# Optimization experiments

Hardware: AMD Instinct MI355X
Metric: run time of the kernel (lower is better)

The kernel has to match this reference:

```python
import jax, jax.numpy as jnp
import numpy as np

NEG_SLOPE = 0.2
EPS = 1e-16  # PyG softmax denominator epsilon


def _gatv2_layer(x, src, dst, n_nodes, W_l, W_r, att, bias):
    """Single-head GATv2Conv (PyG defaults, self loops already in src/dst).
    x: [N, F_in]; src/dst: [E]; W_l/W_r: [F_in, F_out]; att: [F_out]; bias: [F_out].
    """
    x_l = x @ W_l                       # source transform [N, F_out]
    x_r = x @ W_r                       # target transform [N, F_out]
    # per-edge attention logit: a^T LeakyReLU(x_l[j] + x_r[i])
    e = jax.nn.leaky_relu(x_l[src] + x_r[dst], NEG_SLOPE) @ att  # [E]
    # softmax over incoming edges of each destination node
    e_max = jax.ops.segment_max(e, dst, num_segments=n_nodes)    # [N]
    ex = jnp.exp(e - e_max[dst])                                  # [E]
    denom = jax.ops.segment_sum(ex, dst, num_segments=n_nodes)   # [N]
    alpha = ex / (denom[dst] + EPS)                               # [E]
    out = jax.ops.segment_sum(alpha[:, None] * x_l[src], dst, num_segments=n_nodes)
    return out + bias


def setup_inputs() -> dict:
    key = jax.random.key(0)
    N, E = 50000, 800000
    IN, HID, OUT = 128, 64, 64
    ks = jax.random.split(key, 12)
    x = jax.random.normal(ks[0], (N, IN), dtype=jnp.float32)
    edge_index = jax.random.randint(ks[1], (2, E), 0, N, dtype=jnp.int64)
    s1 = float(1.0 / np.sqrt(IN))
    s2 = float(1.0 / np.sqrt(HID))
    return {
        "x": x,
        "edge_index": edge_index,
        "W1_l": jax.random.uniform(ks[2], (IN, HID), jnp.float32, -s1, s1),
        "W1_r": jax.random.uniform(ks[3], (IN, HID), jnp.float32, -s1, s1),
        "att1": jax.random.uniform(ks[4], (HID,), jnp.float32, -s2, s2),
        "b1": jnp.zeros((HID,), jnp.float32),
        "W2_l": jax.random.uniform(ks[5], (HID, OUT), jnp.float32, -s2, s2),
        "W2_r": jax.random.uniform(ks[6], (HID, OUT), jnp.float32, -s2, s2),
        "att2": jax.random.uniform(ks[7], (OUT,), jnp.float32, -s2, s2),
        "b2": jnp.zeros((OUT,), jnp.float32),
    }


def reference(x, edge_index, W1_l, W1_r, att1, b1, W2_l, W2_r, att2, b2):
    n = x.shape[0]
    loop = jnp.arange(n, dtype=edge_index.dtype)
    src = jnp.concatenate([edge_index[0], loop])  # add self loops (PyG default)
    dst = jnp.concatenate([edge_index[1], loop])
    h = _gatv2_layer(x, src, dst, n, W1_l, W1_r, att1, b1)
    h = jax.nn.relu(h)
    out = _gatv2_layer(h, src, dst, n, W2_l, W2_r, att2, b2)
    return out
```

## Files before the change

### kernel.cpp

```cpp
#include <hip/hip_runtime.h>
#include <math.h>

#define NEG_SLOPE 0.2f
#define EPSV 1e-16f
#define NEG_HUGE -1e30f
#define CAP 64
#define GB 2048

typedef short short8 __attribute__((ext_vector_type(8)));
typedef float f32x4 __attribute__((ext_vector_type(4)));
typedef unsigned short u16;


__global__ __launch_bounds__(256) void k_wpack(
        const float* __restrict__ W1l, const float* __restrict__ W1r,
        const float* __restrict__ W2l, const float* __restrict__ W2r,
        u16* __restrict__ w1hi, u16* __restrict__ w1lo,
        u16* __restrict__ w2hi, u16* __restrict__ w2lo,
        int* __restrict__ cnt, u16* __restrict__ csrc, int N, int NP) {
    const int idx = blockIdx.x * 256 + threadIdx.x;
    const int G = gridDim.x * 256;
    const int CN = 8 * NP;
    for (int i = idx; i < CN; i += G) {
        const int cls = i / NP;
        const int r = i - cls * NP;
        const int d = r * 8 + cls;
        cnt[i] = (d < N) ? 1 : 0;
    }
    for (int d = idx; d < N; d += G) csrc[(size_t)d * CAP] = (u16)d;
    const int T1 = 128 * 128, T2 = 64 * 128;
    if (idx >= T1 + T2) return;
    u16 *dhi, *dlo; const float *Wl, *Wr; int li;
    if (idx < T1) { dhi = w1hi; dlo = w1lo; Wl = W1l; Wr = W1r; li = idx; }
    else          { dhi = w2hi; dlo = w2lo; Wl = W2l; Wr = W2r; li = idx - T1; }
    const int j = li & 7, l = (li >> 3) & 63, t = (li >> 9) & 7, c = li >> 12;
    const int k = c * 32 + (l >> 4) * 8 + j;
    const int n = t * 16 + (l & 15);
    const float v = (n < 64) ? Wl[k * 64 + n] : Wr[k * 64 + (n - 64)];
    const unsigned u = __float_as_uint(v);
    dhi[li] = (u16)(u >> 16);
    const float hif = __uint_as_float(u & 0xffff0000u);
    dlo[li] = (u16)(__float_as_uint(v - hif) >> 16);
}

__device__ __forceinline__ void split8(const float* fs, short8& ahi, short8& alo) {
#pragma unroll
    for (int j = 0; j < 8; ++j) {
        const unsigned u = __float_as_uint(fs[j]);
        ahi[j] = (short)(u >> 16);
        const float hif = __uint_as_float(u & 0xffff0000u);
        alo[j] = (short)(__float_as_uint(fs[j] - hif) >> 16);
    }
}

template <int K>
__device__ __forceinline__ void gemm_mfma_tile(const float* __restrict__ X,
                                               const u16* __restrict__ whi,
                                               const u16* __restrict__ wlo,
                                               float* __restrict__ xl,
                                               float* __restrict__ xr,
                                               int N, int tile) {
    const int lane = threadIdx.x & 63;
    const int w = threadIdx.x >> 6;
    const int rowbase = tile * 64 + w * 16;
    const int m = lane & 15, q = lane >> 4;
    int ar = rowbase + m; if (ar > N - 1) ar = N - 1;
    const float* arow = X + (size_t)ar * K + q * 8;
    f32x4 acc[8];
#pragma unroll
    for (int t = 0; t < 8; ++t) acc[t] = (f32x4){0.f, 0.f, 0.f, 0.f};
#pragma unroll
    for (int c = 0; c < K / 32; ++c) {
        const float4 f0 = *(const float4*)(arow + c * 32);
        const float4 f1 = *(const float4*)(arow + c * 32 + 4);
        const float fs[8] = {f0.x, f0.y, f0.z, f0.w, f1.x, f1.y, f1.z, f1.w};
        short8 ahi, alo;
        split8(fs, ahi, alo);
        const u16* bp = whi + ((size_t)(c * 8) * 64 + lane) * 8;
        const u16* bq = wlo + ((size_t)(c * 8) * 64 + lane) * 8;
#pragma unroll
        for (int t = 0; t < 8; ++t) {
            const short8 bhi = *(const short8*)(bp + t * 64 * 8);
            const short8 blo = *(const short8*)(bq + t * 64 * 8);
            acc[t] = __builtin_amdgcn_mfma_f32_16x16x32_bf16(bhi, ahi, acc[t], 0, 0, 0);
            acc[t] = __builtin_amdgcn_mfma_f32_16x16x32_bf16(blo, ahi, acc[t], 0, 0, 0);
            acc[t] = __builtin_amdgcn_mfma_f32_16x16x32_bf16(bhi, alo, acc[t], 0, 0, 0);
        }
    }
    const int row = rowbase + m;
    if (row < N) {
#pragma unroll
        for (int t = 0; t < 8; ++t) {
            const int colb = t * 16 + q * 4;
            float4 v;
            v.x = acc[t][0]; v.y = acc[t][1]; v.z = acc[t][2]; v.w = acc[t][3];
            float* dstp = (t < 4) ? (xl + (size_t)row * 64 + colb)
                                  : (xr + (size_t)row * 64 + (colb - 64));
            *(float4*)dstp = v;
        }
    }
}

__global__ __launch_bounds__(256) void k_build(const int* __restrict__ ei, int E,
                                               int* __restrict__ cnt,
                                               u16* __restrict__ csrc,
                                               int N, int NP) {
    const int cls = blockIdx.x & 7;
    const int stripe = blockIdx.x >> 3;
    const int NS = GB >> 3;
    const int tid = threadIdx.x;
    const int* srcp = ei;
    const int* dstp = ei + E;
    int* cntc = cnt + cls * NP;
    if ((E & 3) == 0) {
        for (int base = stripe * 1024; base < E; base += NS * 1024) {
            const int e4 = base + tid * 4;
            if (e4 < E) {
                const int4 d4 = *(const int4*)(dstp + e4);
                const int4 s4 = *(const int4*)(srcp + e4);
                const int d[4] = {d4.x, d4.y, d4.z, d4.w};
                const int s[4] = {s4.x, s4.y, s4.z, s4.w};
                bool m[4]; int sl[4];
#pragma unroll
                for (int j = 0; j < 4; ++j) {
                    m[j] = (d[j] & 7) == cls;
                    if (m[j]) sl[j] = atomicAdd(&cntc[d[j] >> 3], 1);
                }
#pragma unroll
                for (int j = 0; j < 4; ++j) {
                    if (m[j]) csrc[(size_t)d[j] * CAP + sl[j]] = (u16)s[j];
                }
            }
        }
    } else {
        for (int base = stripe * 256; base < E; base += NS * 256) {
            const int e = base + tid;
            if (e < E) {
                const int dd = dstp[e];
                if ((dd & 7) == cls) {
                    const int ss = srcp[e];
                    const int slot = atomicAdd(&cntc[dd >> 3], 1);
                    csrc[(size_t)dd * CAP + slot] = (u16)ss;
                }
            }
        }
    }
}

template <int K>
__global__ __launch_bounds__(256) void k_gemm(const float* __restrict__ X,
                                              const u16* __restrict__ whi,
                                              const u16* __restrict__ wlo,
                                              float* __restrict__ xl,
                                              float* __restrict__ xr, int N) {
    gemm_mfma_tile<K>(X, whi, wlo, xl, xr, N, blockIdx.x);
}

__global__ __launch_bounds__(256) void k_attn(const float* __restrict__ xl,
                                              const float* xr,
                                              const float* __restrict__ att,
                                              const int* __restrict__ cnt,
                                              const u16* __restrict__ csrc,
                                              const float* __restrict__ bias,
                                              float* out, int N, int NP, int relu) {
    const int lane = threadIdx.x & 63;
    const int g = lane >> 4;
    const int i = lane & 15;
    const int dst = blockIdx.x * 4 + (threadIdx.x >> 6);
    if (dst >= N) return;
    const float4 xrv = *(const float4*)(xr + (size_t)dst * 64 + i * 4);
    const float4 aw  = *(const float4*)(att + i * 4);
    const int deg = cnt[(dst & 7) * NP + (dst >> 3)];
    const int sidx = (int)csrc[(size_t)dst * CAP + ((lane < deg) ? lane : 0)];
    float l = 0.0f;
    float4 acc = {0.0f, 0.0f, 0.0f, 0.0f};
    for (int t = 0; t < deg; t += 16) {
        const int s0 = t + g, s1 = t + 4 + g, s2 = t + 8 + g, s3 = t + 12 + g;
        const bool v0 = s0 < deg, v1 = s1 < deg, v2 = s2 < deg, v3 = s3 < deg;
        const int src0 = __shfl(sidx, s0, 64);
        const int src1 = __shfl(sidx, s1, 64);
        const int src2 = __shfl(sidx, s2, 64);
        const int src3 = __shfl(sidx, s3, 64);
        const float4 va = *(const float4*)(xl + (size_t)src0 * 64 + i * 4);
        const float4 vb = *(const float4*)(xl + (size_t)src1 * 64 + i * 4);
        const float4 vc = *(const float4*)(xl + (size_t)src2 * 64 + i * 4);
        const float4 vd = *(const float4*)(xl + (size_t)src3 * 64 + i * 4);
        float t0, p0, p1, p2, p3;
        t0 = va.x + xrv.x; t0 = fmaxf(t0, NEG_SLOPE * t0); p0 = aw.x * t0;
        t0 = va.y + xrv.y; t0 = fmaxf(t0, NEG_SLOPE * t0); p0 = fmaf(aw.y, t0, p0);
        t0 = va.z + xrv.z; t0 = fmaxf(t0, NEG_SLOPE * t0); p0 = fmaf(aw.z, t0, p0);
        t0 = va.w + xrv.w; t0 = fmaxf(t0, NEG_SLOPE * t0); p0 = fmaf(aw.w, t0, p0);
        t0 = vb.x + xrv.x; t0 = fmaxf(t0, NEG_SLOPE * t0); p1 = aw.x * t0;
        t0 = vb.y + xrv.y; t0 = fmaxf(t0, NEG_SLOPE * t0); p1 = fmaf(aw.y, t0, p1);
        t0 = vb.z + xrv.z; t0 = fmaxf(t0, NEG_SLOPE * t0); p1 = fmaf(aw.z, t0, p1);
        t0 = vb.w + xrv.w; t0 = fmaxf(t0, NEG_SLOPE * t0); p1 = fmaf(aw.w, t0, p1);
        t0 = vc.x + xrv.x; t0 = fmaxf(t0, NEG_SLOPE * t0); p2 = aw.x * t0;
        t0 = vc.y + xrv.y; t0 = fmaxf(t0, NEG_SLOPE * t0); p2 = fmaf(aw.y, t0, p2);
        t0 = vc.z + xrv.z; t0 = fmaxf(t0, NEG_SLOPE * t0); p2 = fmaf(aw.z, t0, p2);
        t0 = vc.w + xrv.w; t0 = fmaxf(t0, NEG_SLOPE * t0); p2 = fmaf(aw.w, t0, p2);
        t0 = vd.x + xrv.x; t0 = fmaxf(t0, NEG_SLOPE * t0); p3 = aw.x * t0;
        t0 = vd.y + xrv.y; t0 = fmaxf(t0, NEG_SLOPE * t0); p3 = fmaf(aw.y, t0, p3);
        t0 = vd.z + xrv.z; t0 = fmaxf(t0, NEG_SLOPE * t0); p3 = fmaf(aw.z, t0, p3);
        t0 = vd.w + xrv.w; t0 = fmaxf(t0, NEG_SLOPE * t0); p3 = fmaf(aw.w, t0, p3);
        p0 += __shfl_xor(p0, 1, 64); p1 += __shfl_xor(p1, 1, 64);
        p2 += __shfl_xor(p2, 1, 64); p3 += __shfl_xor(p3, 1, 64);
        p0 += __shfl_xor(p0, 2, 64); p1 += __shfl_xor(p1, 2, 64);
        p2 += __shfl_xor(p2, 2, 64); p3 += __shfl_xor(p3, 2, 64);
        p0 += __shfl_xor(p0, 4, 64); p1 += __shfl_xor(p1, 4, 64);
        p2 += __shfl_xor(p2, 4, 64); p3 += __shfl_xor(p3, 4, 64);
        p0 += __shfl_xor(p0, 8, 64); p1 += __shfl_xor(p1, 8, 64);
        p2 += __shfl_xor(p2, 8, 64); p3 += __shfl_xor(p3, 8, 64);
        const float d0 = __expf(v0 ? p0 : NEG_HUGE);
        const float d1 = __expf(v1 ? p1 : NEG_HUGE);
        const float d2 = __expf(v2 ? p2 : NEG_HUGE);
        const float d3 = __expf(v3 ? p3 : NEG_HUGE);
        l += (d0 + d1) + (d2 + d3);
        acc.x = fmaf(d0, va.x, fmaf(d1, vb.x, fmaf(d2, vc.x, fmaf(d3, vd.x, acc.x))));
        acc.y = fmaf(d0, va.y, fmaf(d1, vb.y, fmaf(d2, vc.y, fmaf(d3, vd.y, acc.y))));
        acc.z = fmaf(d0, va.z, fmaf(d1, vb.z, fmaf(d2, vc.z, fmaf(d3, vd.z, acc.z))));
        acc.w = fmaf(d0, va.w, fmaf(d1, vb.w, fmaf(d2, vc.w, fmaf(d3, vd.w, acc.w))));
    }
#pragma unroll
    for (int o = 16; o <= 32; o <<= 1) {
        l     += __shfl_xor(l, o, 64);
        acc.x += __shfl_xor(acc.x, o, 64);
        acc.y += __shfl_xor(acc.y, o, 64);
        acc.z += __shfl_xor(acc.z, o, 64);
        acc.w += __shfl_xor(acc.w, o, 64);
    }
    if (g == 0) {
        const float4 bv = *(const float4*)(bias + i * 4);
        const float inv = 1.0f / (l + EPSV);
        float4 r;
        r.x = fmaf(acc.x, inv, bv.x);
        r.y = fmaf(acc.y, inv, bv.y);
        r.z = fmaf(acc.z, inv, bv.z);
        r.w = fmaf(acc.w, inv, bv.w);
        if (relu) {
            r.x = fmaxf(r.x, 0.0f); r.y = fmaxf(r.y, 0.0f);
            r.z = fmaxf(r.z, 0.0f); r.w = fmaxf(r.w, 0.0f);
        }
        *(float4*)(out + (size_t)dst * 64 + i * 4) = r;
    }
}


extern "C" void kernel_launch(void* const* d_in, const int* in_sizes, int n_in,
                              void* d_out, int out_size, void* d_ws, size_t ws_size,
                              hipStream_t stream) {
    const float* x    = (const float*)d_in[0];
    const int*   ei   = (const int*)d_in[1];
    const float* W1l  = (const float*)d_in[2];
    const float* W1r  = (const float*)d_in[3];
    const float* att1 = (const float*)d_in[4];
    const float* b1   = (const float*)d_in[5];
    const float* W2l  = (const float*)d_in[6];
    const float* W2r  = (const float*)d_in[7];
    const float* att2 = (const float*)d_in[8];
    const float* b2   = (const float*)d_in[9];

    const int N  = in_sizes[0] / 128;
    const int E  = in_sizes[1] / 2;
    const int NP = (((N + 7) >> 3) + 31) & ~31;

    int* wsi   = (int*)d_ws;
    int* cnt   = wsi;
    u16* csrc  = (u16*)(cnt + 8 * NP);
    u16* w1hi  = csrc + (size_t)N * CAP;
    u16* w1lo  = w1hi + 16384;
    u16* w2hi  = w1lo + 16384;
    u16* w2lo  = w2hi + 8192;
    float* buf1 = (float*)(w2lo + 8192);
    float* buf2 = buf1 + (size_t)N * 64;
    float* fout = (float*)d_out;

    const dim3 b256(256);
    const int gGemm = (N + 63) / 64;
    const int gAttn = (N + 3) / 4;

    k_wpack<<<256, b256, 0, stream>>>(
        W1l, W1r, W2l, W2r, w1hi, w1lo, w2hi, w2lo, cnt, csrc, N, NP);

    k_build<<<GB, b256, 0, stream>>>(ei, E, cnt, csrc, N, NP);

    k_gemm<128><<<gGemm, b256, 0, stream>>>(x, w1hi, w1lo, fout, buf1, N);

    k_attn<<<gAttn, b256, 0, stream>>>(fout, buf1, att1, cnt, csrc, b1, buf2, N, NP, 1);

    k_gemm<64><<<gGemm, b256, 0, stream>>>(buf2, w2hi, w2lo, buf1, fout, N);
    k_attn<<<gAttn, b256, 0, stream>>>(buf1, fout, att2, cnt, csrc, b2, fout, N, NP, 0);
}
```

Baseline: 224.6 us.

## Store x_l in bf16 and fuse edge histogram build with first GEMM

```diff
diff --git a/kernel.cpp b/kernel.cpp
--- a/kernel.cpp
+++ b/kernel.cpp
@@ -5,12 +5,20 @@
 #define EPSV 1e-16f
 #define NEG_HUGE -1e30f
 #define CAP 64
-#define GB 2048
+#define GH 512
 
 typedef short short8 __attribute__((ext_vector_type(8)));
 typedef float f32x4 __attribute__((ext_vector_type(4)));
 typedef unsigned short u16;
 
+
+__device__ __forceinline__ u16 f2bf(float f) {
+    const unsigned u = __float_as_uint(f);
+    return (u16)((u + 0x7fffu + ((u >> 16) & 1u)) >> 16);
+}
+__device__ __forceinline__ float bf2f(u16 h) {
+    return __uint_as_float(((unsigned)h) << 16);
+}
 
 __global__ __launch_bounds__(256) void k_wpack(
         const float* __restrict__ W1l, const float* __restrict__ W1r,
@@ -57,7 +65,7 @@
 __device__ __forceinline__ void gemm_mfma_tile(const float* __restrict__ X,
                                                const u16* __restrict__ whi,
                                                const u16* __restrict__ wlo,
-                                               float* __restrict__ xl,
+                                               u16* __restrict__ xl,
                                                float* __restrict__ xr,
                                                int N, int tile) {
     const int lane = threadIdx.x & 63;
@@ -92,58 +100,73 @@
 #pragma unroll
         for (int t = 0; t < 8; ++t) {
             const int colb = t * 16 + q * 4;
-            float4 v;
-            v.x = acc[t][0]; v.y = acc[t][1]; v.z = acc[t][2]; v.w = acc[t][3];
-            float* dstp = (t < 4) ? (xl + (size_t)row * 64 + colb)
-                                  : (xr + (size_t)row * 64 + (colb - 64));
-            *(float4*)dstp = v;
+            if (t < 4) {
+                ushort4 hv;
+                hv.x = f2bf(acc[t][0]); hv.y = f2bf(acc[t][1]);
+                hv.z = f2bf(acc[t][2]); hv.w = f2bf(acc[t][3]);
+                *(ushort4*)(xl + (size_t)row * 64 + colb) = hv;
+            } else {
+                float4 v;
+                v.x = acc[t][0]; v.y = acc[t][1]; v.z = acc[t][2]; v.w = acc[t][3];
+                *(float4*)(xr + (size_t)row * 64 + (colb - 64)) = v;
+            }
         }
     }
 }
 
-__global__ __launch_bounds__(256) void k_build(const int* __restrict__ ei, int E,
-                                               int* __restrict__ cnt,
-                                               u16* __restrict__ csrc,
-                                               int N, int NP) {
-    const int cls = blockIdx.x & 7;
-    const int stripe = blockIdx.x >> 3;
-    const int NS = GB >> 3;
-    const int tid = threadIdx.x;
-    const int* srcp = ei;
-    const int* dstp = ei + E;
-    int* cntc = cnt + cls * NP;
-    if ((E & 3) == 0) {
-        for (int base = stripe * 1024; base < E; base += NS * 1024) {
-            const int e4 = base + tid * 4;
-            if (e4 < E) {
-                const int4 d4 = *(const int4*)(dstp + e4);
-                const int4 s4 = *(const int4*)(srcp + e4);
-                const int d[4] = {d4.x, d4.y, d4.z, d4.w};
-                const int s[4] = {s4.x, s4.y, s4.z, s4.w};
-                bool m[4]; int sl[4];
-#pragma unroll
-                for (int j = 0; j < 4; ++j) {
-                    m[j] = (d[j] & 7) == cls;
-                    if (m[j]) sl[j] = atomicAdd(&cntc[d[j] >> 3], 1);
+template <int K>
+__global__ __launch_bounds__(256) void k_hist_gemm(const int* __restrict__ ei, int E,
+                                                   int* __restrict__ cnt,
+                                                   u16* __restrict__ csrc,
+                                                   const float* __restrict__ X,
+                                                   const u16* __restrict__ whi,
+                                                   const u16* __restrict__ wlo,
+                                                   u16* __restrict__ xl,
+                                                   float* __restrict__ xr,
+                                                   int N, int NP) {
+    if ((int)blockIdx.x < GH) {
+        const int cls = blockIdx.x & 7;
+        const int stripe = blockIdx.x >> 3;
+        const int NS = GH >> 3;
+        const int tid = threadIdx.x;
+        const int* srcp = ei;
+        const int* dstp = ei + E;
+        int* cntc = cnt + cls * NP;
+        if ((E & 3) == 0) {
+            for (int base = stripe * 1024; base < E; base += NS * 1024) {
+                const int e4 = base + tid * 4;
+                if (e4 < E) {
+                    const int4 d4 = *(const int4*)(dstp + e4);
+                    const int4 s4 = *(const int4*)(srcp + e4);
+                    const int d[4] = {d4.x, d4.y, d4.z, d4.w};
+                    const int s[4] = {s4.x, s4.y, s4.z, s4.w};
+                    bool m[4]; int sl[4];
+#pragma unroll
+                    for (int j = 0; j < 4; ++j) {
+                        m[j] = (d[j] & 7) == cls;
+                        if (m[j]) sl[j] = atomicAdd(&cntc[d[j] >> 3], 1);
+                    }
+#pragma unroll
+                    for (int j = 0; j < 4; ++j) {
+                        if (m[j]) csrc[(size_t)d[j] * CAP + sl[j]] = (u16)s[j];
+                    }
                 }
-#pragma unroll
-                for (int j = 0; j < 4; ++j) {
-                    if (m[j]) csrc[(size_t)d[j] * CAP + sl[j]] = (u16)s[j];
+            }
+        } else {
+            for (int base = stripe * 256; base < E; base += NS * 256) {
+                const int e = base + tid;
+                if (e < E) {
+                    const int dd = dstp[e];
+                    if ((dd & 7) == cls) {
+                        const int ss = srcp[e];
+                        const int slot = atomicAdd(&cntc[dd >> 3], 1);
+                        csrc[(size_t)dd * CAP + slot] = (u16)ss;
+                    }
                 }
             }
         }
     } else {
-        for (int base = stripe * 256; base < E; base += NS * 256) {
-            const int e = base + tid;
-            if (e < E) {
-                const int dd = dstp[e];
-                if ((dd & 7) == cls) {
-                    const int ss = srcp[e];
-                    const int slot = atomicAdd(&cntc[dd >> 3], 1);
-                    csrc[(size_t)dd * CAP + slot] = (u16)ss;
-                }
-            }
-        }
+        gemm_mfma_tile<K>(X, whi, wlo, xl, xr, N, blockIdx.x - GH);
     }
 }
 
@@ -151,12 +174,12 @@
 __global__ __launch_bounds__(256) void k_gemm(const float* __restrict__ X,
                                               const u16* __restrict__ whi,
                                               const u16* __restrict__ wlo,
-                                              float* __restrict__ xl,
+                                              u16* __restrict__ xl,
                                               float* __restrict__ xr, int N) {
     gemm_mfma_tile<K>(X, whi, wlo, xl, xr, N, blockIdx.x);
 }
 
-__global__ __launch_bounds__(256) void k_attn(const float* __restrict__ xl,
+__global__ __launch_bounds__(256) void k_attn(const u16* __restrict__ xl,
                                               const float* xr,
                                               const float* __restrict__ att,
                                               const int* __restrict__ cnt,
@@ -181,10 +204,15 @@
         const int src1 = __shfl(sidx, s1, 64);
         const int src2 = __shfl(sidx, s2, 64);
         const int src3 = __shfl(sidx, s3, 64);
-        const float4 va = *(const float4*)(xl + (size_t)src0 * 64 + i * 4);
-        const float4 vb = *(const float4*)(xl + (size_t)src1 * 64 + i * 4);
-        const float4 vc = *(const float4*)(xl + (size_t)src2 * 64 + i * 4);
-        const float4 vd = *(const float4*)(xl + (size_t)src3 * 64 + i * 4);
+        const ushort4 ua = *(const ushort4*)(xl + (size_t)src0 * 64 + i * 4);
+        const ushort4 ub = *(const ushort4*)(xl + (size_t)src1 * 64 + i * 4);
+        const ushort4 uc = *(const ushort4*)(xl + (size_t)src2 * 64 + i * 4);
+        const ushort4 ud = *(const ushort4*)(xl + (size_t)src3 * 64 + i * 4);
+        float4 va, vb, vc, vd;
+        va.x = bf2f(ua.x); va.y = bf2f(ua.y); va.z = bf2f(ua.z); va.w = bf2f(ua.w);
+        vb.x = bf2f(ub.x); vb.y = bf2f(ub.y); vb.z = bf2f(ub.z); vb.w = bf2f(ub.w);
+        vc.x = bf2f(uc.x); vc.y = bf2f(uc.y); vc.z = bf2f(uc.z); vc.w = bf2f(uc.w);
+        vd.x = bf2f(ud.x); vd.y = bf2f(ud.y); vd.z = bf2f(ud.z); vd.w = bf2f(ud.w);
         float t0, p0, p1, p2, p3;
         t0 = va.x + xrv.x; t0 = fmaxf(t0, NEG_SLOPE * t0); p0 = aw.x * t0;
         t0 = va.y + xrv.y; t0 = fmaxf(t0, NEG_SLOPE * t0); p0 = fmaf(aw.y, t0, p0);
@@ -278,15 +306,16 @@
     const int gGemm = (N + 63) / 64;
     const int gAttn = (N + 3) / 4;
 
-    k_wpack<<<256, b256, 0, stream>>>(
+    k_wpack<<<96, b256, 0, stream>>>(
         W1l, W1r, W2l, W2r, w1hi, w1lo, w2hi, w2lo, cnt, csrc, N, NP);
 
-    k_build<<<GB, b256, 0, stream>>>(ei, E, cnt, csrc, N, NP);
-
-    k_gemm<128><<<gGemm, b256, 0, stream>>>(x, w1hi, w1lo, fout, buf1, N);
-
-    k_attn<<<gAttn, b256, 0, stream>>>(fout, buf1, att1, cnt, csrc, b1, buf2, N, NP, 1);
-
-    k_gemm<64><<<gGemm, b256, 0, stream>>>(buf2, w2hi, w2lo, buf1, fout, N);
-    k_attn<<<gAttn, b256, 0, stream>>>(buf1, fout, att2, cnt, csrc, b2, fout, N, NP, 0);
-}
+    k_hist_gemm<128><<<GH + gGemm, b256, 0, stream>>>(ei, E, cnt, csrc,
+                                                      x, w1hi, w1lo,
+                                                      (u16*)fout, buf1, N, NP);
+    k_attn<<<gAttn, b256, 0, stream>>>((const u16*)fout, buf1, att1, cnt, csrc, b1,
+                                       buf2, N, NP, 1);
+
+    k_gemm<64><<<gGemm, b256, 0, stream>>>(buf2, w2hi, w2lo, (u16*)buf1, fout, N);
+    k_attn<<<gAttn, b256, 0, stream>>>((const u16*)buf1, fout, att2, cnt, csrc, b2,
+                                       fout, N, NP, 0);
+}
```

Result: faster. 205.0 us (-8.8%).
